# Performance work log

Hardware: AMD Instinct MI355X
Metric: run time of the kernel (lower is better)

Reference implementation:

```python
import jax, jax.numpy as jnp
import numpy as np

D_PAIR, C, N_HEAD = 128, 32, 4
B, N = 1, 256
MASK_INF = 1e9


def layernorm(x, w, b, eps=1e-5):
    mu = jnp.mean(x, axis=-1, keepdims=True)
    var = jnp.var(x, axis=-1, keepdims=True)
    return (x - mu) * jax.lax.rsqrt(var + eps) * w + b


def setup_inputs() -> dict:
    key = jax.random.key(0)
    ks = jax.random.split(key, 10)
    d, h, c = D_PAIR, N_HEAD, C
    s = 0.02
    return {
        "Z_raw": jax.random.normal(ks[0], (B, N, N, d), jnp.float32),
        "Z_mask": jnp.ones((B, N, N), jnp.float32),
        "ln_w": jnp.ones((d,), jnp.float32),
        "ln_b": jnp.zeros((d,), jnp.float32),
        "w_b": jax.random.normal(ks[1], (d, h), jnp.float32) * s,   # pair-bias proj, no bias
        "wq": jax.random.normal(ks[2], (d, h, c), jnp.float32) * s,
        "wk": jax.random.normal(ks[3], (d, h, c), jnp.float32) * s,
        "wv": jax.random.normal(ks[4], (d, h, c), jnp.float32) * s,
        "wg": jax.random.normal(ks[5], (d, h, c), jnp.float32) * s,
        "bg": jnp.ones((h, c), jnp.float32),                        # AF2 gating bias init = 1
        "wo": jax.random.normal(ks[6], (h, c, d), jnp.float32) * s, # last_bias_fuse: no bias here
        "out_bias": jnp.zeros((d,), jnp.float32),
    }


def reference(Z_raw, Z_mask, ln_w, ln_b, w_b, wq, wk, wv, wg, bg, wo, out_bias):
    # Z_raw: [B, I, J, d] pair tensor; attention over J for each row I.
    Z = layernorm(Z_raw, ln_w, ln_b)
    # triangle bias: [B, I, J, h] -> broadcast per-head bias [B, 1, h, q, k]
    tri_b = jnp.einsum("bqkd,dh->bhqk", Z, w_b)[:, None]
    # mask bias over key dim: [B, I, 1, 1, K]
    mask_b = (MASK_INF * (Z_mask - 1.0))[:, :, None, None, :]
    scale = C ** -0.5
    q = jnp.einsum("bijd,dhc->bijhc", Z, wq) * scale
    k = jnp.einsum("bijd,dhc->bijhc", Z, wk)
    v = jnp.einsum("bijd,dhc->bijhc", Z, wv)
    logits = jnp.einsum("biqhc,bikhc->bihqk", q, k) + mask_b + tri_b
    a = jax.nn.softmax(logits, axis=-1)
    o = jnp.einsum("bihqk,bikhc->biqhc", a, v)
    g = jax.nn.sigmoid(jnp.einsum("bijd,dhc->bijhc", Z, wg) + bg)
    o = o * g
    out = jnp.einsum("biqhc,hcd->biqd", o, wo)
    # bias_dropout_add with all-ones dropout mask, inference mode -> plain add
    return out + out_bias + Z_raw
```

## Files before the change

### kernel.cpp

```cpp
#include <hip/hip_runtime.h>


#define NDIM 256
#define HDIM 4
#define QK_SCALE 0.17677669529663687f

typedef unsigned short u16;
typedef unsigned int u32;
typedef __attribute__((ext_vector_type(8))) short bf16x8;
typedef __attribute__((ext_vector_type(4))) float f32x4;

__device__ __forceinline__ float bf2f_lo(u32 u){ union {u32 i; float f;} v; v.i = u<<16; return v.f; }
__device__ __forceinline__ float bf2f_hi(u32 u){ union {u32 i; float f;} v; v.i = u & 0xffff0000u; return v.f; }
__device__ __forceinline__ float bf2f(u16 u){ union {u32 i; float f;} v; v.i = ((u32)u)<<16; return v.f; }
__device__ __forceinline__ u16 f2bf(float f){
    union {u32 i; float f;} v; v.f = f;
    u32 r = v.i + 0x7fffu + ((v.i>>16)&1u);
    return (u16)(r>>16);
}
__device__ __forceinline__ u32 pack2(float a, float b){ return ((u32)f2bf(a)) | (((u32)f2bf(b))<<16); }

template<bool BF16> __device__ __forceinline__ float ld1(const void* p, long i){
    if (BF16) return bf2f(((const u16*)p)[i]);
    return ((const float*)p)[i];
}
template<bool BF16> __device__ __forceinline__ float2 ld2f(const void* p, long pair){
    if (BF16){ u32 u = ((const u32*)p)[pair]; return make_float2(bf2f_lo(u), bf2f_hi(u)); }
    return ((const float2*)p)[pair];
}
template<bool BF16> __device__ __forceinline__ void st1(void* p, long i, float v){
    if (BF16) ((u16*)p)[i] = f2bf(v);
    else      ((float*)p)[i] = v;
}
template<bool BF16> __device__ __forceinline__ void load8f(const void* p, long idx, float* f){
    if (BF16){
        uint4 u = *(const uint4*)((const u16*)p + idx);
        f[0]=bf2f_lo(u.x); f[1]=bf2f_hi(u.x); f[2]=bf2f_lo(u.y); f[3]=bf2f_hi(u.y);
        f[4]=bf2f_lo(u.z); f[5]=bf2f_hi(u.z); f[6]=bf2f_lo(u.w); f[7]=bf2f_hi(u.w);
    } else {
        const float4* q = (const float4*)((const float*)p + idx);
        float4 a = q[0], b = q[1];
        f[0]=a.x; f[1]=a.y; f[2]=a.z; f[3]=a.w; f[4]=b.x; f[5]=b.y; f[6]=b.z; f[7]=b.w;
    }
}
__device__ __forceinline__ bf16x8 pack8(const float* f){
    bf16x8 r;
    #pragma unroll
    for (int j = 0; j < 8; j++) r[j] = (short)f2bf(f[j]);
    return r;
}
__device__ __forceinline__ void unpack16(uint4 u, u16* e){
    e[0]=(u16)u.x; e[1]=(u16)(u.x>>16); e[2]=(u16)u.y; e[3]=(u16)(u.y>>16);
    e[4]=(u16)u.z; e[5]=(u16)(u.z>>16); e[6]=(u16)u.w; e[7]=(u16)(u.w>>16);
}
__device__ __forceinline__ bool mask_is_bf16(const void* mask){
    return ((const u32*)mask)[0] == 0x3F803F80u;
}

template<bool BF16>
__global__ __launch_bounds__(256, 2) void proj_kernel(
    const void* __restrict__ zraw, const void* __restrict__ mask,
    const void* __restrict__ lnw, const void* __restrict__ lnb,
    const void* __restrict__ wb,
    const void* __restrict__ wq, const void* __restrict__ wk,
    const void* __restrict__ wv, const void* __restrict__ wg,
    const void* __restrict__ bg,
    u16* __restrict__ trib,
    u16* __restrict__ qb, u16* __restrict__ kb,
    u16* __restrict__ vb, u16* __restrict__ gb)
{
    if (mask_is_bf16(mask) != BF16) return;
    __shared__ u16 zA[128*136];
    __shared__ u16 wS[128*136];
    __shared__ u16 wbS[16*136];
    __shared__ float muS[128], rsS[128], lnS[128], lbS[128];
    int t = threadIdx.x, w = t >> 6, L = t & 63, lm = L & 15, lq = L >> 4;
    int pos0 = blockIdx.x * 128;
    int i = pos0 >> 8, j0 = pos0 & 255;

    if (t < 128){ lnS[t] = ld1<BF16>(lnw, t); lbS[t] = ld1<BF16>(lnb, t); }
    for (int idx = t; idx < 16*136; idx += 256) wbS[idx] = 0;
    if (BF16){
        const uint4* zp = (const uint4*)((const u16*)zraw + (long)pos0*128);
        #pragma unroll
        for (int n = 0; n < 8; n++){
            int g = t + n*256;
            int row = g >> 4, c0 = (g & 15)*8;
            *(uint4*)&zA[row*136 + c0] = zp[g];
        }
    } else {
        const float4* zp = (const float4*)((const float*)zraw + (long)pos0*128);
        #pragma unroll
        for (int n = 0; n < 16; n++){
            int g = t + n*256;
            int row = g >> 5, c0 = (g & 31)*4;
            float4 f = zp[g];
            *(u32*)&zA[row*136 + c0]     = pack2(f.x, f.y);
            *(u32*)&zA[row*136 + c0 + 2] = pack2(f.z, f.w);
        }
    }
    __syncthreads();
    {
        int row = t >> 1, half = t & 1;
        float s = 0.f, ss = 0.f;
        #pragma unroll
        for (int n = 0; n < 8; n++){
            bf16x8 v = *(const bf16x8*)&zA[row*136 + half*64 + n*8];
            #pragma unroll
            for (int j = 0; j < 8; j++){ float x = bf2f((u16)v[j]); s += x; ss += x*x; }
        }
        s += __shfl_xor(s, 1); ss += __shfl_xor(ss, 1);
        if (half == 0){
            float mu = s*(1.f/128.f);
            float var = ss*(1.f/128.f) - mu*mu;
            muS[row] = mu; rsS[row] = rsqrtf(var + 1e-5f);
        }
    }
    for (int idx = t; idx < 512; idx += 256){
        int d = idx >> 2, n = idx & 3;
        wbS[n*136 + d] = f2bf(ld1<BF16>(wb, idx));
    }
    __syncthreads();
    #pragma unroll 8
    for (int n = 0; n < 64; n++){
        int e = t + n*256;
        int row = e >> 7, col = e & 127;
        float x = bf2f(zA[row*136 + col]);
        zA[row*136 + col] = f2bf((x - muS[row])*rsS[row]*lnS[col] + lbS[col]);
    }
    __syncthreads();
    bf16x8 aA[2][4];
    #pragma unroll
    for (int Mt = 0; Mt < 2; Mt++)
        #pragma unroll
        for (int ks = 0; ks < 4; ks++)
            aA[Mt][ks] = *(const bf16x8*)&zA[((2*w + Mt)*16 + lm)*136 + ks*32 + lq*8];
    f32x4 zero = {0.f,0.f,0.f,0.f};
    {
        bf16x8 bB[4];
        #pragma unroll
        for (int ks = 0; ks < 4; ks++)
            bB[ks] = *(const bf16x8*)&wbS[lm*136 + ks*32 + lq*8];
        #pragma unroll
        for (int Mt = 0; Mt < 2; Mt++){
            f32x4 a = zero;
            #pragma unroll
            for (int ks = 0; ks < 4; ks++)
                a = __builtin_amdgcn_mfma_f32_16x16x32_bf16(aA[Mt][ks], bB[ks], a, 0, 0, 0);
            if (lm < 4){
                #pragma unroll
                for (int r = 0; r < 4; r++){
                    int row = (2*w + Mt)*16 + lq*4 + r;
                    trib[((long)(lm*NDIM + i))*NDIM + j0 + row] = f2bf(a[r]);
                }
            }
        }
    }
    const void* Ws[4] = {wq, wk, wv, wg};
    u16* Os[4] = {qb, kb, vb, gb};
    for (int m = 0; m < 4; m++){
        __syncthreads();
        if (BF16){
            const uint4* wp = (const uint4*)Ws[m];
            #pragma unroll
            for (int n = 0; n < 8; n++){
                int g = t + n*256;
                int d = g >> 4, n0 = (g & 15)*8;
                u16 e[8]; unpack16(wp[g], e);
                #pragma unroll
                for (int q2 = 0; q2 < 8; q2++) wS[(n0 + q2)*136 + d] = e[q2];
            }
        } else {
            const float* wp = (const float*)Ws[m];
            #pragma unroll
            for (int n = 0; n < 64; n++){
                int g = t + n*256;
                int d = g >> 7, nc = g & 127;
                wS[nc*136 + d] = f2bf(wp[g]);
            }
        }
        __syncthreads();
        f32x4 acc[2][8];
        #pragma unroll
        for (int Mt = 0; Mt < 2; Mt++)
            #pragma unroll
            for (int Nt = 0; Nt < 8; Nt++) acc[Mt][Nt] = zero;
        #pragma unroll
        for (int ks = 0; ks < 4; ks++){
            bf16x8 bB[8];
            #pragma unroll
            for (int Nt = 0; Nt < 8; Nt++)
                bB[Nt] = *(const bf16x8*)&wS[(Nt*16 + lm)*136 + ks*32 + lq*8];
            #pragma unroll
            for (int Mt = 0; Mt < 2; Mt++)
                #pragma unroll
                for (int Nt = 0; Nt < 8; Nt++)
                    acc[Mt][Nt] = __builtin_amdgcn_mfma_f32_16x16x32_bf16(aA[Mt][ks], bB[Nt], acc[Mt][Nt], 0, 0, 0);
        }
        u16* outp = Os[m];
        #pragma unroll
        for (int Nt = 0; Nt < 8; Nt++){
            int n = Nt*16 + lm;
            int hh = n >> 5, c = n & 31;
            float bgv = (m == 3) ? ld1<BF16>(bg, n) : 0.f;
            #pragma unroll
            for (int Mt = 0; Mt < 2; Mt++)
                #pragma unroll
                for (int r = 0; r < 4; r++){
                    float v = acc[Mt][Nt][r];
                    if (m == 0) v *= QK_SCALE;
                    if (m == 3) v = 1.f/(1.f + __expf(-(v + bgv)));
                    int row = (2*w + Mt)*16 + lq*4 + r;
                    outp[((long)(i*HDIM + hh)*NDIM + (j0 + row))*32 + c] = f2bf(v);
                }
        }
    }
}

template<bool BF16>
__global__ __launch_bounds__(256, 2) void attn_kernel(
    const void* __restrict__ mask,
    const u16* __restrict__ qb, const u16* __restrict__ kb,
    const u16* __restrict__ vb, const u16* __restrict__ gb,
    const u16* __restrict__ trib, u16* __restrict__ obuf)
{
    if (mask_is_bf16(mask) != BF16) return;
    __shared__ u16 kS[256*40];
    __shared__ u16 vS[32*264];
    __shared__ u16 pT[4][32*72];
    __shared__ float mrow[256];
    int b = blockIdx.x;
    int i = b >> 3, h = (b >> 1) & 3, half = b & 1;
    int t = threadIdx.x, w = t >> 6, L = t & 63, lm = L & 15, lq = L >> 4;
    long base = (long)(i*HDIM + h)*NDIM*32;

    const uint4* kp = (const uint4*)(kb + base);
    const uint4* vp = (const uint4*)(vb + base);
    #pragma unroll
    for (int n = 0; n < 4; n++){
        int g = t + n*256;
        int j = g >> 2, c0 = (g & 3)*8;
        *(uint4*)&kS[j*40 + c0] = kp[g];
        u16 e[8]; unpack16(vp[g], e);
        #pragma unroll
        for (int q2 = 0; q2 < 8; q2++)
            vS[(j >> 3)*264 + (c0 + q2)*8 + (j & 7)] = e[q2];
    }
    mrow[t] = 1e9f*(ld1<BF16>(mask, i*NDIM + t) - 1.f);
    int q0 = half*128 + w*32;
    bf16x8 qA[2];
    #pragma unroll
    for (int Mt = 0; Mt < 2; Mt++)
        qA[Mt] = *(const bf16x8*)(qb + base + (long)(q0 + Mt*16 + lm)*32 + lq*8);
    __syncthreads();

    const u16* trq = trib + (long)h*NDIM*NDIM;
    f32x4 zero = {0.f,0.f,0.f,0.f};
    u32 Spk[2][4][8];
    float mS[2][4];
    #pragma unroll
    for (int Mt = 0; Mt < 2; Mt++)
        #pragma unroll
        for (int r = 0; r < 4; r++) mS[Mt][r] = -3e38f;

    u16 trc[2][4][2], trn[2][4][2];
    #pragma unroll
    for (int Mt = 0; Mt < 2; Mt++)
        #pragma unroll
        for (int r = 0; r < 4; r++)
            #pragma unroll
            for (int hf = 0; hf < 2; hf++)
                trc[Mt][r][hf] = trq[(long)(q0 + Mt*16 + lq*4 + r)*NDIM + hf*16 + lm];
    for (int kt = 0; kt < 8; kt++){
        if (kt < 7){
            #pragma unroll
            for (int Mt = 0; Mt < 2; Mt++)
                #pragma unroll
                for (int r = 0; r < 4; r++)
                    #pragma unroll
                    for (int hf = 0; hf < 2; hf++)
                        trn[Mt][r][hf] = trq[(long)(q0 + Mt*16 + lq*4 + r)*NDIM + (kt+1)*32 + hf*16 + lm];
        }
        bf16x8 kB0 = *(const bf16x8*)&kS[(kt*32 + lm)*40 + lq*8];
        bf16x8 kB1 = *(const bf16x8*)&kS[(kt*32 + 16 + lm)*40 + lq*8];
        float mb0 = mrow[kt*32 + lm], mb1 = mrow[kt*32 + 16 + lm];
        #pragma unroll
        for (int Mt = 0; Mt < 2; Mt++){
            f32x4 S0 = __builtin_amdgcn_mfma_f32_16x16x32_bf16(qA[Mt], kB0, zero, 0, 0, 0);
            f32x4 S1 = __builtin_amdgcn_mfma_f32_16x16x32_bf16(qA[Mt], kB1, zero, 0, 0, 0);
            #pragma unroll
            for (int r = 0; r < 4; r++){
                float x0 = S0[r] + mb0 + bf2f(trc[Mt][r][0]);
                float x1 = S1[r] + mb1 + bf2f(trc[Mt][r][1]);
                mS[Mt][r] = fmaxf(mS[Mt][r], fmaxf(x0, x1));
                Spk[Mt][r][kt] = pack2(x0, x1);
            }
        }
        #pragma unroll
        for (int Mt = 0; Mt < 2; Mt++)
            #pragma unroll
            for (int r = 0; r < 4; r++){
                trc[Mt][r][0] = trn[Mt][r][0];
                trc[Mt][r][1] = trn[Mt][r][1];
            }
    }
    #pragma unroll
    for (int Mt = 0; Mt < 2; Mt++)
        #pragma unroll
        for (int r = 0; r < 4; r++){
            float m = mS[Mt][r];
            #pragma unroll
            for (int off = 1; off <= 8; off <<= 1) m = fmaxf(m, __shfl_xor(m, off));
            mS[Mt][r] = m;
        }

    float lsum[2][4] = {{0.f,0.f,0.f,0.f},{0.f,0.f,0.f,0.f}};
    f32x4 O[2][2];
    O[0][0] = zero; O[0][1] = zero; O[1][0] = zero; O[1][1] = zero;
    u16* myp = pT[w];
    #pragma unroll
    for (int ch = 0; ch < 4; ch++){
        #pragma unroll
        for (int Mt = 0; Mt < 2; Mt++)
            #pragma unroll
            for (int r = 0; r < 4; r++){
                int qr = Mt*16 + lq*4 + r;
                #pragma unroll
                for (int kk = 0; kk < 2; kk++){
                    u32 sp = Spk[Mt][r][ch*2 + kk];
                    float p0 = __expf(bf2f_lo(sp) - mS[Mt][r]);
                    float p1 = __expf(bf2f_hi(sp) - mS[Mt][r]);
                    lsum[Mt][r] += p0 + p1;
                    myp[qr*72 + kk*32 + lm]      = f2bf(p0);
                    myp[qr*72 + kk*32 + 16 + lm] = f2bf(p1);
                }
            }
        #pragma unroll
        for (int ks = 0; ks < 2; ks++){
            int kbi = ch*8 + ks*4 + lq;
            bf16x8 vB0 = *(const bf16x8*)&vS[kbi*264 + lm*8];
            bf16x8 vB1 = *(const bf16x8*)&vS[kbi*264 + (16 + lm)*8];
            #pragma unroll
            for (int Mt = 0; Mt < 2; Mt++){
                bf16x8 pA = *(const bf16x8*)&myp[(Mt*16 + lm)*72 + ks*32 + lq*8];
                O[Mt][0] = __builtin_amdgcn_mfma_f32_16x16x32_bf16(pA, vB0, O[Mt][0], 0, 0, 0);
                O[Mt][1] = __builtin_amdgcn_mfma_f32_16x16x32_bf16(pA, vB1, O[Mt][1], 0, 0, 0);
            }
        }
    }
    #pragma unroll
    for (int Mt = 0; Mt < 2; Mt++)
        #pragma unroll
        for (int r = 0; r < 4; r++){
            float l = lsum[Mt][r];
            #pragma unroll
            for (int off = 1; off <= 8; off <<= 1) l += __shfl_xor(l, off);
            lsum[Mt][r] = l;
        }
    #pragma unroll
    for (int Mt = 0; Mt < 2; Mt++)
        #pragma unroll
        for (int r = 0; r < 4; r++){
            float inv = 1.f/lsum[Mt][r];
            int q = q0 + Mt*16 + lq*4 + r;
            long ob = (long)(i*NDIM + q)*128 + h*32;
            obuf[ob + lm]      = f2bf(O[Mt][0][r]*inv*bf2f(gb[base + (long)q*32 + lm]));
            obuf[ob + 16 + lm] = f2bf(O[Mt][1][r]*inv*bf2f(gb[base + (long)q*32 + 16 + lm]));
        }
}

template<bool BF16>
__global__ __launch_bounds__(256, 2) void outproj_mfma_kernel(
    const void* __restrict__ mask, const u16* __restrict__ obuf,
    const void* __restrict__ wo, const void* __restrict__ obias,
    const void* __restrict__ zraw, void* __restrict__ out)
{
    if (mask_is_bf16(mask) != BF16) return;
    __shared__ u16 woT[128*136];
    int t = threadIdx.x, w = t >> 6, L = t & 63;
    int lm = L & 15, lq = L >> 4;
    for (int idx = t; idx < 16384; idx += 256){
        int hc = idx >> 7, d = idx & 127;
        woT[d*136 + hc] = f2bf(ld1<BF16>(wo, (long)hc*128 + d));
    }
    __syncthreads();
    int pos0 = blockIdx.x*128 + w*32;
    bf16x8 aA[2][4];
    #pragma unroll
    for (int Mt = 0; Mt < 2; Mt++)
        #pragma unroll
        for (int ks = 0; ks < 4; ks++)
            aA[Mt][ks] = *(const bf16x8*)&obuf[((long)(pos0 + Mt*16 + lm))*128 + ks*32 + lq*8];
    f32x4 zero = {0.f,0.f,0.f,0.f};
    f32x4 acc[2][8];
    #pragma unroll
    for (int Mt = 0; Mt < 2; Mt++)
        #pragma unroll
        for (int Nt = 0; Nt < 8; Nt++) acc[Mt][Nt] = zero;
    #pragma unroll
    for (int ks = 0; ks < 4; ks++){
        bf16x8 bB[8];
        #pragma unroll
        for (int Nt = 0; Nt < 8; Nt++)
            bB[Nt] = *(const bf16x8*)&woT[(Nt*16 + lm)*136 + ks*32 + lq*8];
        #pragma unroll
        for (int Mt = 0; Mt < 2; Mt++)
            #pragma unroll
            for (int Nt = 0; Nt < 8; Nt++)
                acc[Mt][Nt] = __builtin_amdgcn_mfma_f32_16x16x32_bf16(aA[Mt][ks], bB[Nt], acc[Mt][Nt], 0, 0, 0);
    }
    float ob[8];
    #pragma unroll
    for (int Nt = 0; Nt < 8; Nt++) ob[Nt] = ld1<BF16>(obias, Nt*16 + lm);
    #pragma unroll
    for (int Mt = 0; Mt < 2; Mt++)
        #pragma unroll
        for (int Nt = 0; Nt < 8; Nt++)
            #pragma unroll
            for (int r = 0; r < 4; r++){
                long pos = pos0 + Mt*16 + lq*4 + r;
                int d = Nt*16 + lm;
                float v = acc[Mt][Nt][r] + ob[Nt] + ld1<BF16>(zraw, pos*128 + d);
                st1<BF16>(out, pos*128 + d, v);
            }
}

template<bool BF16>
__global__ __launch_bounds__(256) void ln_tri_kernel(
    const void* __restrict__ zraw, const void* __restrict__ mask,
    const void* __restrict__ lnw, const void* __restrict__ lnb,
    const void* __restrict__ wb, u16* __restrict__ trib)
{
    if (mask_is_bf16(mask) != BF16) return;
    int wave = threadIdx.x >> 6;
    int lane = threadIdx.x & 63;
    int pos = blockIdx.x * 4 + wave;
    float2 f = ld2f<BF16>(zraw, (long)pos*64 + lane);
    float x0 = f.x, x1 = f.y;
    float s = x0 + x1, ss = x0*x0 + x1*x1;
    #pragma unroll
    for (int off = 32; off; off >>= 1){ s += __shfl_xor(s, off); ss += __shfl_xor(ss, off); }
    float mean = s * (1.0f/128.0f);
    float var  = ss * (1.0f/128.0f) - mean*mean;
    float rstd = rsqrtf(var + 1e-5f);
    int d0 = lane*2;
    float y0 = (x0 - mean)*rstd*ld1<BF16>(lnw, d0)   + ld1<BF16>(lnb, d0);
    float y1 = (x1 - mean)*rstd*ld1<BF16>(lnw, d0+1) + ld1<BF16>(lnb, d0+1);
    int i = pos >> 8, j = pos & 255;
    #pragma unroll
    for (int hh = 0; hh < 4; hh++){
        float tp = y0*ld1<BF16>(wb, d0*4 + hh) + y1*ld1<BF16>(wb, (d0+1)*4 + hh);
        #pragma unroll
        for (int off = 32; off; off >>= 1) tp += __shfl_xor(tp, off);
        if (lane == 0) trib[((long)(hh*NDIM + i))*NDIM + j] = f2bf(tp);
    }
}

template<bool BF16>
__global__ __launch_bounds__(256, 2) void attn_mfma_kernel(
    const void* __restrict__ zraw, const void* __restrict__ mask,
    const void* __restrict__ lnw, const void* __restrict__ lnb,
    const void* __restrict__ wq, const void* __restrict__ wk,
    const void* __restrict__ wv, const void* __restrict__ wg,
    const void* __restrict__ bg, const u16* __restrict__ trib,
    u16* __restrict__ obuf)
{
    if (mask_is_bf16(mask) != BF16) return;
    __shared__ u16 wT[32*136];
    __shared__ u16 kS[256*40];
    __shared__ u16 vT[32*264];
    __shared__ u16 pT[4*64*40];
    __shared__ float mrow[256];
    __shared__ float lnS[128], lbS[128];

    int i = blockIdx.x >> 2, h = blockIdx.x & 3;
    int t = threadIdx.x, w = t >> 6, L = t & 63;
    int lm = L & 15, lq = L >> 4;
    mrow[t] = 1e9f*(ld1<BF16>(mask, i*NDIM + t) - 1.0f);
    if (t < 128) lnS[t] = ld1<BF16>(lnw, t);
    else         lbS[t-128] = ld1<BF16>(lnb, t-128);
    __syncthreads();

    int q0 = w*64;
    float zf[4][4][8];
    float s[4] = {0,0,0,0}, ss[4] = {0,0,0,0};
    #pragma unroll
    for (int Mt = 0; Mt < 4; Mt++){
        long row = (long)(i*NDIM + q0 + Mt*16 + lm);
        #pragma unroll
        for (int ks = 0; ks < 4; ks++){
            load8f<BF16>(zraw, row*128 + ks*32 + lq*8, zf[Mt][ks]);
            #pragma unroll
            for (int j = 0; j < 8; j++){ float x = zf[Mt][ks][j]; s[Mt] += x; ss[Mt] += x*x; }
        }
    }
    #pragma unroll
    for (int Mt = 0; Mt < 4; Mt++){
        s[Mt]  += __shfl_xor(s[Mt], 16);  s[Mt]  += __shfl_xor(s[Mt], 32);
        ss[Mt] += __shfl_xor(ss[Mt], 16); ss[Mt] += __shfl_xor(ss[Mt], 32);
    }
    bf16x8 zA[4][4];
    #pragma unroll
    for (int Mt = 0; Mt < 4; Mt++){
        float mean = s[Mt]*(1.f/128.f);
        float var  = ss[Mt]*(1.f/128.f) - mean*mean;
        float rstd = rsqrtf(var + 1e-5f);
        #pragma unroll
        for (int ks = 0; ks < 4; ks++){
            float tmp[8];
            #pragma unroll
            for (int j = 0; j < 8; j++){
                int col = ks*32 + lq*8 + j;
                tmp[j] = (zf[Mt][ks][j] - mean)*rstd*lnS[col] + lbS[col];
            }
            zA[Mt][ks] = pack8(tmp);
        }
    }
    u16* myp = pT + w*2560;
    f32x4 zero = {0.f, 0.f, 0.f, 0.f};
    auto stageW = [&](const void* W){
        for (int idx = t; idx < 4096; idx += 256){
            int c = idx >> 7, d = idx & 127;
            wT[c*136 + d] = f2bf(ld1<BF16>(W, (long)(d*4 + h)*32 + c));
        }
    };
    auto projA = [&](f32x4 (&acc)[4][2]){
        bf16x8 bB[2][4];
        #pragma unroll
        for (int Nt = 0; Nt < 2; Nt++)
            #pragma unroll
            for (int ks = 0; ks < 4; ks++)
                bB[Nt][ks] = *(const bf16x8*)&wT[(Nt*16 + lm)*136 + ks*32 + lq*8];
        #pragma unroll
        for (int Mt = 0; Mt < 4; Mt++)
            #pragma unroll
            for (int Nt = 0; Nt < 2; Nt++){
                f32x4 a = zero;
                #pragma unroll
                for (int ks = 0; ks < 4; ks++)
                    a = __builtin_amdgcn_mfma_f32_16x16x32_bf16(zA[Mt][ks], bB[Nt][ks], a, 0, 0, 0);
                acc[Mt][Nt] = a;
            }
    };
    f32x4 acc[4][2];
    stageW(wq); __syncthreads();
    projA(acc);
    #pragma unroll
    for (int Mt = 0; Mt < 4; Mt++)
        #pragma unroll
        for (int Nt = 0; Nt < 2; Nt++)
            #pragma unroll
            for (int r = 0; r < 4; r++)
                myp[(Mt*16 + lq*4 + r)*40 + Nt*16 + lm] = f2bf(acc[Mt][Nt][r]*QK_SCALE);
    bf16x8 qA[4];
    #pragma unroll
    for (int Mt = 0; Mt < 4; Mt++)
        qA[Mt] = *(const bf16x8*)&myp[(Mt*16 + lm)*40 + lq*8];
    __syncthreads();
    stageW(wk); __syncthreads();
    projA(acc);
    #pragma unroll
    for (int Mt = 0; Mt < 4; Mt++)
        #pragma unroll
        for (int Nt = 0; Nt < 2; Nt++)
            #pragma unroll
            for (int r = 0; r < 4; r++)
                kS[(q0 + Mt*16 + lq*4 + r)*40 + Nt*16 + lm] = f2bf(acc[Mt][Nt][r]);
    __syncthreads();
    stageW(wv); __syncthreads();
    projA(acc);
    #pragma unroll
    for (int Mt = 0; Mt < 4; Mt++)
        #pragma unroll
        for (int Nt = 0; Nt < 2; Nt++)
            #pragma unroll
            for (int r = 0; r < 4; r++)
                vT[(Nt*16 + lm)*264 + q0 + Mt*16 + lq*4 + r] = f2bf(acc[Mt][Nt][r]);
    __syncthreads();
    stageW(wg); __syncthreads();
    f32x4 gv[4][2];
    projA(gv);
    float bgv0 = ld1<BF16>(bg, h*32 + lm), bgv1 = ld1<BF16>(bg, h*32 + 16 + lm);
    #pragma unroll
    for (int Mt = 0; Mt < 4; Mt++)
        #pragma unroll
        for (int r = 0; r < 4; r++){
            gv[Mt][0][r] = 1.f/(1.f + __expf(-(gv[Mt][0][r] + bgv0)));
            gv[Mt][1][r] = 1.f/(1.f + __expf(-(gv[Mt][1][r] + bgv1)));
        }
    __syncthreads();
    float mS[4][4], lS[4][4];
    f32x4 O[4][2];
    #pragma unroll
    for (int Mt = 0; Mt < 4; Mt++){
        #pragma unroll
        for (int r = 0; r < 4; r++){ mS[Mt][r] = -3e38f; lS[Mt][r] = 0.f; }
        O[Mt][0] = zero; O[Mt][1] = zero;
    }
    const u16* trb = trib + ((long)(h*NDIM + q0))*NDIM;
    for (int kt = 0; kt < 8; kt++){
        bf16x8 kB0 = *(const bf16x8*)&kS[(kt*32 + lm)*40 + lq*8];
        bf16x8 kB1 = *(const bf16x8*)&kS[(kt*32 + 16 + lm)*40 + lq*8];
        f32x4 S[4][2];
        #pragma unroll
        for (int Mt = 0; Mt < 4; Mt++){
            S[Mt][0] = __builtin_amdgcn_mfma_f32_16x16x32_bf16(qA[Mt], kB0, zero, 0, 0, 0);
            S[Mt][1] = __builtin_amdgcn_mfma_f32_16x16x32_bf16(qA[Mt], kB1, zero, 0, 0, 0);
        }
        int k0 = kt*32 + lm;
        float mb0 = mrow[k0], mb1 = mrow[k0 + 16];
        #pragma unroll
        for (int Mt = 0; Mt < 4; Mt++){
            #pragma unroll
            for (int r = 0; r < 4; r++){
                int qrow = Mt*16 + lq*4 + r;
                float x0 = S[Mt][0][r] + mb0 + bf2f(trb[(long)qrow*NDIM + k0]);
                float x1 = S[Mt][1][r] + mb1 + bf2f(trb[(long)qrow*NDIM + k0 + 16]);
                float mx = fmaxf(x0, x1);
                #pragma unroll
                for (int off = 1; off <= 8; off <<= 1) mx = fmaxf(mx, __shfl_xor(mx, off));
                float mnew = fmaxf(mS[Mt][r], mx);
                float al = __expf(mS[Mt][r] - mnew);
                float p0 = __expf(x0 - mnew), p1 = __expf(x1 - mnew);
                float rs = p0 + p1;
                #pragma unroll
                for (int off = 1; off <= 8; off <<= 1) rs += __shfl_xor(rs, off);
                lS[Mt][r] = lS[Mt][r]*al + rs;
                mS[Mt][r] = mnew;
                O[Mt][0][r] *= al; O[Mt][1][r] *= al;
                myp[qrow*40 + lm]      = f2bf(p0);
                myp[qrow*40 + 16 + lm] = f2bf(p1);
            }
        }
        bf16x8 vB0 = *(const bf16x8*)&vT[lm*264 + kt*32 + lq*8];
        bf16x8 vB1 = *(const bf16x8*)&vT[(16 + lm)*264 + kt*32 + lq*8];
        #pragma unroll
        for (int Mt = 0; Mt < 4; Mt++){
            bf16x8 pA = *(const bf16x8*)&myp[(Mt*16 + lm)*40 + lq*8];
            O[Mt][0] = __builtin_amdgcn_mfma_f32_16x16x32_bf16(pA, vB0, O[Mt][0], 0, 0, 0);
            O[Mt][1] = __builtin_amdgcn_mfma_f32_16x16x32_bf16(pA, vB1, O[Mt][1], 0, 0, 0);
        }
    }
    #pragma unroll
    for (int Mt = 0; Mt < 4; Mt++)
        #pragma unroll
        for (int r = 0; r < 4; r++){
            float inv = 1.0f/lS[Mt][r];
            int q = q0 + Mt*16 + lq*4 + r;
            long base = ((long)(i*NDIM + q))*128 + h*32;
            obuf[base + lm]      = f2bf(O[Mt][0][r]*inv*gv[Mt][0][r]);
            obuf[base + 16 + lm] = f2bf(O[Mt][1][r]*inv*gv[Mt][1][r]);
        }
}

extern "C" void kernel_launch(void* const* d_in, const int* in_sizes, int n_in,
                              void* d_out, int out_size, void* d_ws, size_t ws_size,
                              hipStream_t stream)
{
    const void* zraw = d_in[0];
    const void* mask = d_in[1];
    const void* lnw  = d_in[2];
    const void* lnb  = d_in[3];
    const void* wb   = d_in[4];
    const void* wq   = d_in[5];
    const void* wk   = d_in[6];
    const void* wv   = d_in[7];
    const void* wg   = d_in[8];
    const void* bg   = d_in[9];
    const void* wo   = d_in[10];
    const void* obias= d_in[11];

    const size_t MB = 1024*1024;
    u16* trib = (u16*)d_ws;
    size_t need_big = 81*MB;
    bool big = ws_size >= need_big;

    if (big){
        u16* qb   = (u16*)((char*)d_ws + 1*MB);
        u16* kb   = (u16*)((char*)d_ws + 17*MB);
        u16* vb   = (u16*)((char*)d_ws + 33*MB);
        u16* gb   = (u16*)((char*)d_ws + 49*MB);
        u16* obuf = (u16*)((char*)d_ws + 65*MB);
        proj_kernel<true ><<<dim3(512), 256, 0, stream>>>(
            zraw, mask, lnw, lnb, wb, wq, wk, wv, wg, bg, trib, qb, kb, vb, gb);
        proj_kernel<false><<<dim3(512), 256, 0, stream>>>(
            zraw, mask, lnw, lnb, wb, wq, wk, wv, wg, bg, trib, qb, kb, vb, gb);
        attn_kernel<true ><<<dim3(2048), 256, 0, stream>>>(mask, qb, kb, vb, gb, trib, obuf);
        attn_kernel<false><<<dim3(2048), 256, 0, stream>>>(mask, qb, kb, vb, gb, trib, obuf);
        outproj_mfma_kernel<true ><<<dim3(512), 256, 0, stream>>>(mask, obuf, wo, obias, zraw, d_out);
        outproj_mfma_kernel<false><<<dim3(512), 256, 0, stream>>>(mask, obuf, wo, obias, zraw, d_out);
    } else {
        u16* obuf = (u16*)((char*)d_ws + 1*MB);
        ln_tri_kernel<true ><<<dim3(NDIM*NDIM/4), 256, 0, stream>>>(zraw, mask, lnw, lnb, wb, trib);
        ln_tri_kernel<false><<<dim3(NDIM*NDIM/4), 256, 0, stream>>>(zraw, mask, lnw, lnb, wb, trib);
        attn_mfma_kernel<true ><<<dim3(NDIM*HDIM), 256, 0, stream>>>(
            zraw, mask, lnw, lnb, wq, wk, wv, wg, bg, trib, obuf);
        attn_mfma_kernel<false><<<dim3(NDIM*HDIM), 256, 0, stream>>>(
            zraw, mask, lnw, lnb, wq, wk, wv, wg, bg, trib, obuf);
        outproj_mfma_kernel<true ><<<dim3(512), 256, 0, stream>>>(mask, obuf, wo, obias, zraw, d_out);
        outproj_mfma_kernel<false><<<dim3(512), 256, 0, stream>>>(mask, obuf, wo, obias, zraw, d_out);
    }
}
```

Before: 211.9 us.

## Pretranspose weights once, merge dtype launches, use exp2 softmax and transposed bias

Adds a prep kernel that converts and transposes the q/k/v/g, pair-bias and output weights to bf16 once, so the projection and out-projection blocks read B fragments straight from global memory instead of staging them through shared memory every block. Each dtype-specialised kernel pair becomes a single launch that branches at runtime, which cuts the number of launches. The attention kernel folds log2(e) into q, the triangle bias and the mask so it can use exp2. It also reads the triangle bias from a transposed layout, permutes V in shared memory so P can be stored packed, and reuses the K buffer for P to raise occupancy. The out-projection stages its result in shared memory so the residual add uses vectorised, coalesced loads and stores. The cost is an extra launch and weight fragment reads that now go through global memory and cache.

```diff
diff --git a/kernel.cpp b/kernel.cpp
--- a/kernel.cpp
+++ b/kernel.cpp
@@ -4,6 +4,7 @@
 #define NDIM 256
 #define HDIM 4
 #define QK_SCALE 0.17677669529663687f
+#define LOG2E    1.4426950408889634f
 
 typedef unsigned short u16;
 typedef unsigned int u32;
@@ -19,6 +20,7 @@
     return (u16)(r>>16);
 }
 __device__ __forceinline__ u32 pack2(float a, float b){ return ((u32)f2bf(a)) | (((u32)f2bf(b))<<16); }
+__device__ __forceinline__ int sig2(int c){ return ((c&7)<<2) | (c>>3); }
 
 template<bool BF16> __device__ __forceinline__ float ld1(const void* p, long i){
     if (BF16) return bf2f(((const u16*)p)[i]);
@@ -58,28 +60,59 @@
 }
 
 template<bool BF16>
-__global__ __launch_bounds__(256, 2) void proj_kernel(
-    const void* __restrict__ zraw, const void* __restrict__ mask,
+__device__ __forceinline__ void prep_body(
+    const void* wq, const void* wk, const void* wv, const void* wg,
+    const void* wb, const void* wo,
+    u16* __restrict__ wT4, u16* __restrict__ wbT,
+    u16* __restrict__ woP, u16* __restrict__ woL)
+{
+    int id = blockIdx.x*256 + threadIdx.x;
+    int stride = gridDim.x*256;
+    const void* Ws[4] = {wq, wk, wv, wg};
+    for (int idx = id; idx < 4*16384; idx += stride){
+        int m = idx >> 14, r = idx & 16383, n = r >> 7, d = r & 127;
+        wT4[idx] = f2bf(ld1<BF16>(Ws[m], (long)d*128 + n));
+    }
+    for (int idx = id; idx < 2048; idx += stride){
+        int n = idx >> 7, d = idx & 127;
+        wbT[idx] = (n < 4) ? f2bf(ld1<BF16>(wb, (long)d*4 + n)) : (u16)0;
+    }
+    for (int idx = id; idx < 16384; idx += stride){
+        int dout = idx >> 7, hc = idx & 127;
+        int hh = hc >> 5, c = hc & 31;
+        float v = ld1<BF16>(wo, (long)hc*128 + dout);
+        woL[idx] = f2bf(v);
+        woP[dout*128 + hh*32 + sig2(c)] = f2bf(v);
+    }
+}
+
+__global__ __launch_bounds__(256) void prep_kernel(
+    const void* mask, const void* wq, const void* wk, const void* wv,
+    const void* wg, const void* wb, const void* wo,
+    u16* wT4, u16* wbT, u16* woP, u16* woL)
+{
+    if (mask_is_bf16(mask)) prep_body<true >(wq,wk,wv,wg,wb,wo,wT4,wbT,woP,woL);
+    else                    prep_body<false>(wq,wk,wv,wg,wb,wo,wT4,wbT,woP,woL);
+}
+
+template<bool BF16>
+__device__ __forceinline__ void proj_body(
+    const void* __restrict__ zraw,
     const void* __restrict__ lnw, const void* __restrict__ lnb,
-    const void* __restrict__ wb,
-    const void* __restrict__ wq, const void* __restrict__ wk,
-    const void* __restrict__ wv, const void* __restrict__ wg,
+    const u16* __restrict__ wT4, const u16* __restrict__ wbT,
     const void* __restrict__ bg,
     u16* __restrict__ trib,
     u16* __restrict__ qb, u16* __restrict__ kb,
-    u16* __restrict__ vb, u16* __restrict__ gb)
-{
-    if (mask_is_bf16(mask) != BF16) return;
-    __shared__ u16 zA[128*136];
-    __shared__ u16 wS[128*136];
-    __shared__ u16 wbS[16*136];
-    __shared__ float muS[128], rsS[128], lnS[128], lbS[128];
+    u16* __restrict__ vb, u16* __restrict__ gb,
+    u16* __restrict__ zA, float* __restrict__ fS)
+{
+    float* muS = fS;       float* rsS = fS + 128;
+    float* lnS = fS + 256; float* lbS = fS + 384;
     int t = threadIdx.x, w = t >> 6, L = t & 63, lm = L & 15, lq = L >> 4;
     int pos0 = blockIdx.x * 128;
     int i = pos0 >> 8, j0 = pos0 & 255;
 
     if (t < 128){ lnS[t] = ld1<BF16>(lnw, t); lbS[t] = ld1<BF16>(lnb, t); }
-    for (int idx = t; idx < 16*136; idx += 256) wbS[idx] = 0;
     if (BF16){
         const uint4* zp = (const uint4*)((const u16*)zraw + (long)pos0*128);
         #pragma unroll
@@ -116,10 +149,6 @@
             muS[row] = mu; rsS[row] = rsqrtf(var + 1e-5f);
         }
     }
-    for (int idx = t; idx < 512; idx += 256){
-        int d = idx >> 2, n = idx & 3;
-        wbS[n*136 + d] = f2bf(ld1<BF16>(wb, idx));
-    }
     __syncthreads();
     #pragma unroll 8
     for (int n = 0; n < 64; n++){
@@ -140,7 +169,7 @@
         bf16x8 bB[4];
         #pragma unroll
         for (int ks = 0; ks < 4; ks++)
-            bB[ks] = *(const bf16x8*)&wbS[lm*136 + ks*32 + lq*8];
+            bB[ks] = *(const bf16x8*)&wbT[lm*128 + ks*32 + lq*8];
         #pragma unroll
         for (int Mt = 0; Mt < 2; Mt++){
             f32x4 a = zero;
@@ -150,36 +179,15 @@
             if (lm < 4){
                 #pragma unroll
                 for (int r = 0; r < 4; r++){
-                    int row = (2*w + Mt)*16 + lq*4 + r;
-                    trib[((long)(lm*NDIM + i))*NDIM + j0 + row] = f2bf(a[r]);
+                    int k = j0 + (2*w + Mt)*16 + lq*4 + r;
+                    trib[((long)(lm*NDIM + k))*NDIM + i] = f2bf(a[r]*LOG2E);
                 }
             }
         }
     }
-    const void* Ws[4] = {wq, wk, wv, wg};
     u16* Os[4] = {qb, kb, vb, gb};
     for (int m = 0; m < 4; m++){
-        __syncthreads();
-        if (BF16){
-            const uint4* wp = (const uint4*)Ws[m];
-            #pragma unroll
-            for (int n = 0; n < 8; n++){
-                int g = t + n*256;
-                int d = g >> 4, n0 = (g & 15)*8;
-                u16 e[8]; unpack16(wp[g], e);
-                #pragma unroll
-                for (int q2 = 0; q2 < 8; q2++) wS[(n0 + q2)*136 + d] = e[q2];
-            }
-        } else {
-            const float* wp = (const float*)Ws[m];
-            #pragma unroll
-            for (int n = 0; n < 64; n++){
-                int g = t + n*256;
-                int d = g >> 7, nc = g & 127;
-                wS[nc*136 + d] = f2bf(wp[g]);
-            }
-        }
-        __syncthreads();
+        const u16* Wp = wT4 + m*16384;
         f32x4 acc[2][8];
         #pragma unroll
         for (int Mt = 0; Mt < 2; Mt++)
@@ -190,7 +198,7 @@
             bf16x8 bB[8];
             #pragma unroll
             for (int Nt = 0; Nt < 8; Nt++)
-                bB[Nt] = *(const bf16x8*)&wS[(Nt*16 + lm)*136 + ks*32 + lq*8];
+                bB[Nt] = *(const bf16x8*)&Wp[(Nt*16 + lm)*128 + ks*32 + lq*8];
             #pragma unroll
             for (int Mt = 0; Mt < 2; Mt++)
                 #pragma unroll
@@ -199,36 +207,47 @@
         }
         u16* outp = Os[m];
         #pragma unroll
-        for (int Nt = 0; Nt < 8; Nt++){
-            int n = Nt*16 + lm;
-            int hh = n >> 5, c = n & 31;
-            float bgv = (m == 3) ? ld1<BF16>(bg, n) : 0.f;
+        for (int tp = 0; tp < 4; tp++){
+            float bg0 = (m == 3) ? ld1<BF16>(bg, tp*32 + lm)      : 0.f;
+            float bg1 = (m == 3) ? ld1<BF16>(bg, tp*32 + 16 + lm) : 0.f;
             #pragma unroll
             for (int Mt = 0; Mt < 2; Mt++)
                 #pragma unroll
                 for (int r = 0; r < 4; r++){
-                    float v = acc[Mt][Nt][r];
-                    if (m == 0) v *= QK_SCALE;
-                    if (m == 3) v = 1.f/(1.f + __expf(-(v + bgv)));
+                    float v0 = acc[Mt][2*tp][r], v1 = acc[Mt][2*tp + 1][r];
+                    if (m == 0){ v0 *= QK_SCALE*LOG2E; v1 *= QK_SCALE*LOG2E; }
+                    if (m == 3){
+                        v0 = 1.f/(1.f + __expf(-(v0 + bg0)));
+                        v1 = 1.f/(1.f + __expf(-(v1 + bg1)));
+                    }
                     int row = (2*w + Mt)*16 + lq*4 + r;
-                    outp[((long)(i*HDIM + hh)*NDIM + (j0 + row))*32 + c] = f2bf(v);
+                    u32* dst = (u32*)(outp + ((long)(i*HDIM + tp)*NDIM + (j0 + row))*32);
+                    dst[lm] = pack2(v0, v1);
                 }
         }
     }
 }
 
+__global__ __launch_bounds__(256, 3) void proj_kernel(
+    const void* zraw, const void* mask,
+    const void* lnw, const void* lnb,
+    const u16* wT4, const u16* wbT, const void* bg,
+    u16* trib, u16* qb, u16* kb, u16* vb, u16* gb)
+{
+    __shared__ u16 zA[128*136];
+    __shared__ float fS[512];
+    if (mask_is_bf16(mask)) proj_body<true >(zraw, lnw, lnb, wT4, wbT, bg, trib, qb, kb, vb, gb, zA, fS);
+    else                    proj_body<false>(zraw, lnw, lnb, wT4, wbT, bg, trib, qb, kb, vb, gb, zA, fS);
+}
+
 template<bool BF16>
-__global__ __launch_bounds__(256, 2) void attn_kernel(
+__device__ __forceinline__ void attn_body(
     const void* __restrict__ mask,
     const u16* __restrict__ qb, const u16* __restrict__ kb,
     const u16* __restrict__ vb, const u16* __restrict__ gb,
-    const u16* __restrict__ trib, u16* __restrict__ obuf)
-{
-    if (mask_is_bf16(mask) != BF16) return;
-    __shared__ u16 kS[256*40];
-    __shared__ u16 vS[32*264];
-    __shared__ u16 pT[4][32*72];
-    __shared__ float mrow[256];
+    const u16* __restrict__ trib, u16* __restrict__ obuf,
+    u16* __restrict__ kS, u16* __restrict__ vS, float* __restrict__ mrow)
+{
     int b = blockIdx.x;
     int i = b >> 3, h = (b >> 1) & 3, half = b & 1;
     int t = threadIdx.x, w = t >> 6, L = t & 63, lm = L & 15, lq = L >> 4;
@@ -241,12 +260,14 @@
         int g = t + n*256;
         int j = g >> 2, c0 = (g & 3)*8;
         *(uint4*)&kS[j*40 + c0] = kp[g];
+        int jl = j & 31;
+        int jp = (j & ~31) | ((jl & 15) << 1) | (jl >> 4);
         u16 e[8]; unpack16(vp[g], e);
         #pragma unroll
         for (int q2 = 0; q2 < 8; q2++)
-            vS[(j >> 3)*264 + (c0 + q2)*8 + (j & 7)] = e[q2];
-    }
-    mrow[t] = 1e9f*(ld1<BF16>(mask, i*NDIM + t) - 1.f);
+            vS[(jp >> 3)*264 + (c0 + q2)*8 + (jp & 7)] = e[q2];
+    }
+    mrow[t] = (1e9f*LOG2E)*(ld1<BF16>(mask, i*NDIM + t) - 1.f);
     int q0 = half*128 + w*32;
     bf16x8 qA[2];
     #pragma unroll
@@ -254,7 +275,7 @@
         qA[Mt] = *(const bf16x8*)(qb + base + (long)(q0 + Mt*16 + lm)*32 + lq*8);
     __syncthreads();
 
-    const u16* trq = trib + (long)h*NDIM*NDIM;
+    const u16* trT = trib + (long)h*NDIM*NDIM;
     f32x4 zero = {0.f,0.f,0.f,0.f};
     u32 Spk[2][4][8];
     float mS[2][4];
@@ -263,46 +284,30 @@
         #pragma unroll
         for (int r = 0; r < 4; r++) mS[Mt][r] = -3e38f;
 
-    u16 trc[2][4][2], trn[2][4][2];
-    #pragma unroll
-    for (int Mt = 0; Mt < 2; Mt++)
-        #pragma unroll
-        for (int r = 0; r < 4; r++)
-            #pragma unroll
-            for (int hf = 0; hf < 2; hf++)
-                trc[Mt][r][hf] = trq[(long)(q0 + Mt*16 + lq*4 + r)*NDIM + hf*16 + lm];
     for (int kt = 0; kt < 8; kt++){
-        if (kt < 7){
-            #pragma unroll
-            for (int Mt = 0; Mt < 2; Mt++)
-                #pragma unroll
-                for (int r = 0; r < 4; r++)
-                    #pragma unroll
-                    for (int hf = 0; hf < 2; hf++)
-                        trn[Mt][r][hf] = trq[(long)(q0 + Mt*16 + lq*4 + r)*NDIM + (kt+1)*32 + hf*16 + lm];
-        }
         bf16x8 kB0 = *(const bf16x8*)&kS[(kt*32 + lm)*40 + lq*8];
         bf16x8 kB1 = *(const bf16x8*)&kS[(kt*32 + 16 + lm)*40 + lq*8];
         float mb0 = mrow[kt*32 + lm], mb1 = mrow[kt*32 + 16 + lm];
+        uint2 tr0[2], tr1[2];
+        #pragma unroll
+        for (int Mt = 0; Mt < 2; Mt++){
+            tr0[Mt] = *(const uint2*)&trT[((long)(kt*32 + lm))*NDIM + q0 + Mt*16 + lq*4];
+            tr1[Mt] = *(const uint2*)&trT[((long)(kt*32 + 16 + lm))*NDIM + q0 + Mt*16 + lq*4];
+        }
         #pragma unroll
         for (int Mt = 0; Mt < 2; Mt++){
             f32x4 S0 = __builtin_amdgcn_mfma_f32_16x16x32_bf16(qA[Mt], kB0, zero, 0, 0, 0);
             f32x4 S1 = __builtin_amdgcn_mfma_f32_16x16x32_bf16(qA[Mt], kB1, zero, 0, 0, 0);
+            float tv0[4] = {bf2f_lo(tr0[Mt].x), bf2f_hi(tr0[Mt].x), bf2f_lo(tr0[Mt].y), bf2f_hi(tr0[Mt].y)};
+            float tv1[4] = {bf2f_lo(tr1[Mt].x), bf2f_hi(tr1[Mt].x), bf2f_lo(tr1[Mt].y), bf2f_hi(tr1[Mt].y)};
             #pragma unroll
             for (int r = 0; r < 4; r++){
-                float x0 = S0[r] + mb0 + bf2f(trc[Mt][r][0]);
-                float x1 = S1[r] + mb1 + bf2f(trc[Mt][r][1]);
+                float x0 = S0[r] + mb0 + tv0[r];
+                float x1 = S1[r] + mb1 + tv1[r];
                 mS[Mt][r] = fmaxf(mS[Mt][r], fmaxf(x0, x1));
                 Spk[Mt][r][kt] = pack2(x0, x1);
             }
         }
-        #pragma unroll
-        for (int Mt = 0; Mt < 2; Mt++)
-            #pragma unroll
-            for (int r = 0; r < 4; r++){
-                trc[Mt][r][0] = trn[Mt][r][0];
-                trc[Mt][r][1] = trn[Mt][r][1];
-            }
     }
     #pragma unroll
     for (int Mt = 0; Mt < 2; Mt++)
@@ -313,11 +318,13 @@
             for (int off = 1; off <= 8; off <<= 1) m = fmaxf(m, __shfl_xor(m, off));
             mS[Mt][r] = m;
         }
+
+    __syncthreads();
 
     float lsum[2][4] = {{0.f,0.f,0.f,0.f},{0.f,0.f,0.f,0.f}};
     f32x4 O[2][2];
     O[0][0] = zero; O[0][1] = zero; O[1][0] = zero; O[1][1] = zero;
-    u16* myp = pT[w];
+    u16* myp = kS + w*2304;
     #pragma unroll
     for (int ch = 0; ch < 4; ch++){
         #pragma unroll
@@ -328,11 +335,10 @@
                 #pragma unroll
                 for (int kk = 0; kk < 2; kk++){
                     u32 sp = Spk[Mt][r][ch*2 + kk];
-                    float p0 = __expf(bf2f_lo(sp) - mS[Mt][r]);
-                    float p1 = __expf(bf2f_hi(sp) - mS[Mt][r]);
+                    float p0 = __builtin_amdgcn_exp2f(bf2f_lo(sp) - mS[Mt][r]);
+                    float p1 = __builtin_amdgcn_exp2f(bf2f_hi(sp) - mS[Mt][r]);
                     lsum[Mt][r] += p0 + p1;
-                    myp[qr*72 + kk*32 + lm]      = f2bf(p0);
-                    myp[qr*72 + kk*32 + 16 + lm] = f2bf(p1);
+                    *(u32*)&myp[qr*72 + kk*32 + 2*lm] = pack2(p0, p1);
                 }
             }
         #pragma unroll
@@ -363,34 +369,42 @@
         for (int r = 0; r < 4; r++){
             float inv = 1.f/lsum[Mt][r];
             int q = q0 + Mt*16 + lq*4 + r;
-            long ob = (long)(i*NDIM + q)*128 + h*32;
-            obuf[ob + lm]      = f2bf(O[Mt][0][r]*inv*bf2f(gb[base + (long)q*32 + lm]));
-            obuf[ob + 16 + lm] = f2bf(O[Mt][1][r]*inv*bf2f(gb[base + (long)q*32 + 16 + lm]));
-        }
+            float g0 = bf2f(gb[base + (long)q*32 + lm]);
+            float g1 = bf2f(gb[base + (long)q*32 + 16 + lm]);
+            u32* dst = (u32*)(obuf + (long)(i*NDIM + q)*128 + h*32);
+            dst[lm] = pack2(O[Mt][0][r]*inv*g0, O[Mt][1][r]*inv*g1);
+        }
+}
+
+__global__ __launch_bounds__(256, 4) void attn_kernel(
+    const void* mask, const u16* qb, const u16* kb,
+    const u16* vb, const u16* gb, const u16* trib, u16* obuf)
+{
+    __shared__ u16 kS[256*40];
+    __shared__ u16 vS[32*264];
+    __shared__ float mrow[256];
+    if (mask_is_bf16(mask)) attn_body<true >(mask, qb, kb, vb, gb, trib, obuf, kS, vS, mrow);
+    else                    attn_body<false>(mask, qb, kb, vb, gb, trib, obuf, kS, vS, mrow);
 }
 
 template<bool BF16>
-__global__ __launch_bounds__(256, 2) void outproj_mfma_kernel(
-    const void* __restrict__ mask, const u16* __restrict__ obuf,
-    const void* __restrict__ wo, const void* __restrict__ obias,
-    const void* __restrict__ zraw, void* __restrict__ out)
-{
-    if (mask_is_bf16(mask) != BF16) return;
-    __shared__ u16 woT[128*136];
+__device__ __forceinline__ void outproj_body(
+    const u16* __restrict__ obuf, const u16* __restrict__ woT,
+    const void* __restrict__ obias, const void* __restrict__ zraw,
+    void* __restrict__ out,
+    u16* __restrict__ oT, float* __restrict__ obS)
+{
     int t = threadIdx.x, w = t >> 6, L = t & 63;
     int lm = L & 15, lq = L >> 4;
-    for (int idx = t; idx < 16384; idx += 256){
-        int hc = idx >> 7, d = idx & 127;
-        woT[d*136 + hc] = f2bf(ld1<BF16>(wo, (long)hc*128 + d));
-    }
-    __syncthreads();
-    int pos0 = blockIdx.x*128 + w*32;
+    if (t < 128) obS[t] = ld1<BF16>(obias, t);
+    int pos0 = blockIdx.x*128;
+    int r0 = w*32;
     bf16x8 aA[2][4];
     #pragma unroll
     for (int Mt = 0; Mt < 2; Mt++)
         #pragma unroll
         for (int ks = 0; ks < 4; ks++)
-            aA[Mt][ks] = *(const bf16x8*)&obuf[((long)(pos0 + Mt*16 + lm))*128 + ks*32 + lq*8];
+            aA[Mt][ks] = *(const bf16x8*)&obuf[((long)(pos0 + r0 + Mt*16 + lm))*128 + ks*32 + lq*8];
     f32x4 zero = {0.f,0.f,0.f,0.f};
     f32x4 acc[2][8];
     #pragma unroll
@@ -402,27 +416,71 @@
         bf16x8 bB[8];
         #pragma unroll
         for (int Nt = 0; Nt < 8; Nt++)
-            bB[Nt] = *(const bf16x8*)&woT[(Nt*16 + lm)*136 + ks*32 + lq*8];
+            bB[Nt] = *(const bf16x8*)&woT[(Nt*16 + lm)*128 + ks*32 + lq*8];
         #pragma unroll
         for (int Mt = 0; Mt < 2; Mt++)
             #pragma unroll
             for (int Nt = 0; Nt < 8; Nt++)
                 acc[Mt][Nt] = __builtin_amdgcn_mfma_f32_16x16x32_bf16(aA[Mt][ks], bB[Nt], acc[Mt][Nt], 0, 0, 0);
     }
-    float ob[8];
-    #pragma unroll
-    for (int Nt = 0; Nt < 8; Nt++) ob[Nt] = ld1<BF16>(obias, Nt*16 + lm);
     #pragma unroll
     for (int Mt = 0; Mt < 2; Mt++)
         #pragma unroll
         for (int Nt = 0; Nt < 8; Nt++)
             #pragma unroll
-            for (int r = 0; r < 4; r++){
-                long pos = pos0 + Mt*16 + lq*4 + r;
-                int d = Nt*16 + lm;
-                float v = acc[Mt][Nt][r] + ob[Nt] + ld1<BF16>(zraw, pos*128 + d);
-                st1<BF16>(out, pos*128 + d, v);
-            }
+            for (int r = 0; r < 4; r++)
+                oT[(r0 + Mt*16 + lq*4 + r)*136 + Nt*16 + lm] = f2bf(acc[Mt][Nt][r]);
+    __syncthreads();
+    if (BF16){
+        const uint4* zp = (const uint4*)((const u16*)zraw + (long)pos0*128);
+        uint4* op = (uint4*)((u16*)out + (long)pos0*128);
+        #pragma unroll
+        for (int n = 0; n < 8; n++){
+            int g = t + n*256;
+            int row = g >> 4, c0 = (g & 15)*8;
+            uint4 ov = *(const uint4*)&oT[row*136 + c0];
+            uint4 zv = zp[g];
+            u16 oe[8], ze[8]; unpack16(ov, oe); unpack16(zv, ze);
+            float v[8];
+            #pragma unroll
+            for (int j = 0; j < 8; j++) v[j] = bf2f(oe[j]) + obS[c0 + j] + bf2f(ze[j]);
+            uint4 res;
+            res.x = pack2(v[0], v[1]); res.y = pack2(v[2], v[3]);
+            res.z = pack2(v[4], v[5]); res.w = pack2(v[6], v[7]);
+            op[g] = res;
+        }
+    } else {
+        const float4* zp = (const float4*)((const float*)zraw + (long)pos0*128);
+        float4* op = (float4*)((float*)out + (long)pos0*128);
+        #pragma unroll
+        for (int n = 0; n < 8; n++){
+            int g = t + n*256;
+            int row = g >> 4, c0 = (g & 15)*8;
+            uint4 ov = *(const uint4*)&oT[row*136 + c0];
+            u16 oe[8]; unpack16(ov, oe);
+            float4 z0 = zp[2*g], z1 = zp[2*g + 1];
+            float4 r0v, r1v;
+            r0v.x = bf2f(oe[0]) + obS[c0+0] + z0.x;
+            r0v.y = bf2f(oe[1]) + obS[c0+1] + z0.y;
+            r0v.z = bf2f(oe[2]) + obS[c0+2] + z0.z;
+            r0v.w = bf2f(oe[3]) + obS[c0+3] + z0.w;
+            r1v.x = bf2f(oe[4]) + obS[c0+4] + z1.x;
+            r1v.y = bf2f(oe[5]) + obS[c0+5] + z1.y;
+            r1v.z = bf2f(oe[6]) + obS[c0+6] + z1.z;
+            r1v.w = bf2f(oe[7]) + obS[c0+7] + z1.w;
+            op[2*g] = r0v; op[2*g + 1] = r1v;
+        }
+    }
+}
+
+__global__ __launch_bounds__(256, 3) void outproj_kernel(
+    const void* mask, const u16* obuf, const u16* woT,
+    const void* obias, const void* zraw, void* out)
+{
+    __shared__ u16 oT[128*136];
+    __shared__ float obS[128];
+    if (mask_is_bf16(mask)) outproj_body<true >(obuf, woT, obias, zraw, out, oT, obS);
+    else                    outproj_body<false>(obuf, woT, obias, zraw, out, oT, obS);
 }
 
 template<bool BF16>
@@ -670,25 +728,28 @@
     const void* wo   = d_in[10];
     const void* obias= d_in[11];
 
+    const size_t KB = 1024;
     const size_t MB = 1024*1024;
     u16* trib = (u16*)d_ws;
+    u16* wT4  = (u16*)((char*)d_ws + 512*KB);
+    u16* woP  = (u16*)((char*)d_ws + 640*KB);
+    u16* woL  = (u16*)((char*)d_ws + 672*KB);
+    u16* wbT  = (u16*)((char*)d_ws + 704*KB);
     size_t need_big = 81*MB;
     bool big = ws_size >= need_big;
 
+    prep_kernel<<<dim3(128), 256, 0, stream>>>(mask, wq, wk, wv, wg, wb, wo,
+                                               wT4, wbT, woP, woL);
     if (big){
         u16* qb   = (u16*)((char*)d_ws + 1*MB);
         u16* kb   = (u16*)((char*)d_ws + 17*MB);
         u16* vb   = (u16*)((char*)d_ws + 33*MB);
         u16* gb   = (u16*)((char*)d_ws + 49*MB);
         u16* obuf = (u16*)((char*)d_ws + 65*MB);
-        proj_kernel<true ><<<dim3(512), 256, 0, stream>>>(
-            zraw, mask, lnw, lnb, wb, wq, wk, wv, wg, bg, trib, qb, kb, vb, gb);
-        proj_kernel<false><<<dim3(512), 256, 0, stream>>>(
-            zraw, mask, lnw, lnb, wb, wq, wk, wv, wg, bg, trib, qb, kb, vb, gb);
-        attn_kernel<true ><<<dim3(2048), 256, 0, stream>>>(mask, qb, kb, vb, gb, trib, obuf);
-        attn_kernel<false><<<dim3(2048), 256, 0, stream>>>(mask, qb, kb, vb, gb, trib, obuf);
-        outproj_mfma_kernel<true ><<<dim3(512), 256, 0, stream>>>(mask, obuf, wo, obias, zraw, d_out);
-        outproj_mfma_kernel<false><<<dim3(512), 256, 0, stream>>>(mask, obuf, wo, obias, zraw, d_out);
+        proj_kernel<<<dim3(512), 256, 0, stream>>>(
+            zraw, mask, lnw, lnb, wT4, wbT, bg, trib, qb, kb, vb, gb);
+        attn_kernel<<<dim3(2048), 256, 0, stream>>>(mask, qb, kb, vb, gb, trib, obuf);
+        outproj_kernel<<<dim3(512), 256, 0, stream>>>(mask, obuf, woP, obias, zraw, d_out);
     } else {
         u16* obuf = (u16*)((char*)d_ws + 1*MB);
         ln_tri_kernel<true ><<<dim3(NDIM*NDIM/4), 256, 0, stream>>>(zraw, mask, lnw, lnb, wb, trib);
@@ -697,7 +758,6 @@
             zraw, mask, lnw, lnb, wq, wk, wv, wg, bg, trib, obuf);
         attn_mfma_kernel<false><<<dim3(NDIM*HDIM), 256, 0, stream>>>(
             zraw, mask, lnw, lnb, wq, wk, wv, wg, bg, trib, obuf);
-        outproj_mfma_kernel<true ><<<dim3(512), 256, 0, stream>>>(mask, obuf, wo, obias, zraw, d_out);
-        outproj_mfma_kernel<false><<<dim3(512), 256, 0, stream>>>(mask, obuf, wo, obias, zraw, d_out);
-    }
-}
+        outproj_kernel<<<dim3(512), 256, 0, stream>>>(mask, obuf, woL, obias, zraw, d_out);
+    }
+}
```

After: 305.1 us. 44.0% more time.
